# Kernel optimization log

Hardware: AMD Instinct MI355X
Metric: run time of the kernel (lower is better)

Reference implementation:

```python
import jax, jax.numpy as jnp
import numpy as np

G = 8            # tile grid (8x8)
BINS = 256
CLIP_LIMIT = 4.0
H = W = 4096


def setup_inputs() -> dict:
    key = jax.random.key(0)
    k1, k2 = jax.random.split(key)
    img = jax.random.uniform(k1, (3, H, W), dtype=jnp.float32)
    # torch code draws alpha ~ U(0.5, 1.0) per tile; we pass raw U(0,1) and rescale inside
    alphas = jax.random.uniform(k2, (G * G,), dtype=jnp.float32)
    return {"img": img, "alphas": alphas}


def _to_tiles(x, hs, ws):
    # [h, w] -> [G*G, hs, ws]
    return x.reshape(G, hs, G, ws).transpose(0, 2, 1, 3).reshape(G * G, hs, ws)


def _from_tiles(t, h, w, hs, ws):
    # [G*G, hs, ws] -> [h, w]
    return t.reshape(G, G, hs, ws).transpose(0, 2, 1, 3).reshape(h, w)


def reference(img, alphas):
    c, h, w = img.shape
    hs, ws = h // G, w // G
    n_tiles = G * G
    alpha = (0.5 + 0.5 * alphas)[:, None, None]  # U(0.5,1) per tile

    lum = jnp.mean(img, axis=0)                  # [h, w]
    tiles = _to_tiles(lum, hs, ws)               # [64, hs, ws]

    # per-tile 256-bin histogram over [0,1] (torch.histc semantics: v=1 -> last bin)
    bin_idx = jnp.clip((tiles * BINS).astype(jnp.int32), 0, BINS - 1)
    flat_idx = (jnp.arange(n_tiles, dtype=jnp.int32)[:, None, None] * BINS + bin_idx).reshape(-1)
    hist = jax.ops.segment_sum(
        jnp.ones(flat_idx.shape, jnp.float32), flat_idx, num_segments=n_tiles * BINS
    ).reshape(n_tiles, BINS)

    # clip + uniform redistribution of excess
    cl = float(max(1, int(CLIP_LIMIT * hs * ws / BINS)))
    excess = jnp.sum(jnp.maximum(hist - cl, 0.0), axis=1, keepdims=True)
    hist = jnp.minimum(hist, cl) + excess / BINS

    cdf = jnp.cumsum(hist, axis=1)
    cdf = cdf / cdf[:, -1:]                      # [64, 256]

    tmin = tiles.min(axis=(1, 2), keepdims=True)
    tmax = tiles.max(axis=(1, 2), keepdims=True)
    valid = tmin < tmax                          # [64, 1, 1]

    norm = (tiles - tmin) / jnp.where(valid, tmax - tmin, 1.0)
    idx = jnp.clip((norm * 255.0).astype(jnp.int32), 0, 255)
    enhanced = cdf[jnp.arange(n_tiles)[:, None, None], idx]   # gather remap
    enhanced = alpha * enhanced + (1.0 - alpha) * tiles

    enh_full = _from_tiles(enhanced, h, w, hs, ws)            # [h, w]
    valid_full = _from_tiles(jnp.broadcast_to(valid, (n_tiles, hs, ws)), h, w, hs, ws)

    # per-channel color ratio: img/lum where lum > 1e-5 else 1 (safe division)
    nz = lum > 1e-5
    safe_lum = jnp.where(nz, lum, 1.0)
    ratio = jnp.where(nz[None], img / safe_lum[None], 1.0)    # [3, h, w]

    out = jnp.where(valid_full[None], enh_full[None] * ratio, img)
    return jnp.clip(out, 0.0, 1.0)
```

## Files before the change

kernel.cpp:

```cpp
#include <hip/hip_runtime.h>

#define HH 4096
#define WW 4096
#define TS 512
#define NBINS 256
#define NT 64
#define NCHUNK 32
#define NBLK (NT * NCHUNK)
#define PLANE (HH * WW)

typedef float vf4 __attribute__((ext_vector_type(4)));

__device__ __forceinline__ float wred_min(float v) {
#pragma unroll
    for (int o = 32; o > 0; o >>= 1) v = fminf(v, __shfl_down(v, o, 64));
    return v;
}
__device__ __forceinline__ float wred_max(float v) {
#pragma unroll
    for (int o = 32; o > 0; o >>= 1) v = fmaxf(v, __shfl_down(v, o, 64));
    return v;
}
__device__ __forceinline__ float wred_sum(float v) {
#pragma unroll
    for (int o = 32; o > 0; o >>= 1) v += __shfl_down(v, o, 64);
    return v;
}


#define HIST_LANE(comp)                                              \
    {                                                                \
        float l = (a.comp + b.comp + c.comp) / 3.0f;                 \
        vmin = fminf(vmin, l);                                       \
        vmax = fmaxf(vmax, l);                                       \
        int bb = (int)(l * 256.0f);                                  \
        bb = bb < 0 ? 0 : (bb > 255 ? 255 : bb);                     \
        atomicAdd(&sh[bb], 1u);                                      \
    }

__global__ __launch_bounds__(256) void k_hist_p(const float* __restrict__ img,
                                                unsigned* __restrict__ part,
                                                float* __restrict__ pmin,
                                                float* __restrict__ pmax) {
    __shared__ unsigned sh0[NBINS], sh1[NBINS];
    __shared__ float smin[4], smax[4];
    int tid = threadIdx.x;
    sh0[tid] = 0u;
    sh1[tid] = 0u;
    __syncthreads();

    unsigned* sh = ((tid >> 6) & 1) ? sh1 : sh0;

    int bx = blockIdx.x;
    int t = bx >> 5;
    int chunk = bx & 31;
    int row0 = (t >> 3) * TS + chunk * 16;
    int cb4 = (t & 7) * (TS / 4);

    const float4* p0 = (const float4*)(img);
    const float4* p1 = (const float4*)(img + PLANE);
    const float4* p2 = (const float4*)(img + 2 * PLANE);

    int colv = tid & 127;
    int rsub = tid >> 7;
    float vmin = 1e30f, vmax = -1e30f;

#pragma unroll
    for (int it = 0; it < 8; ++it) {
        int r = row0 + (it << 1) + rsub;
        size_t idx4 = (size_t)r * (WW / 4) + cb4 + colv;
        float4 a = p0[idx4];
        float4 b = p1[idx4];
        float4 c = p2[idx4];
        HIST_LANE(x)
        HIST_LANE(y)
        HIST_LANE(z)
        HIST_LANE(w)
    }

    float wmn = wred_min(vmin), wmx = wred_max(vmax);
    if ((tid & 63) == 0) { smin[tid >> 6] = wmn; smax[tid >> 6] = wmx; }
    __syncthreads();
    if (tid == 0) {
        pmin[bx] = fminf(fminf(smin[0], smin[1]), fminf(smin[2], smin[3]));
        pmax[bx] = fmaxf(fmaxf(smax[0], smax[1]), fmaxf(smax[2], smax[3]));
    }
    part[(size_t)bx * NBINS + tid] = sh0[tid] + sh1[tid];
}

__global__ __launch_bounds__(256) void k_cdf_p(const unsigned* __restrict__ part,
                                               const float* __restrict__ pmin,
                                               const float* __restrict__ pmax,
                                               const float* __restrict__ alphas,
                                               float* __restrict__ cdfa,
                                               float* __restrict__ params) {
    __shared__ float wtot[4];
    __shared__ float wsums[4];
    __shared__ float sminmax[2];
    int t = blockIdx.x, tid = threadIdx.x;

    float h = 0.0f;
#pragma unroll
    for (int c = 0; c < NCHUNK; ++c)
        h += (float)part[((size_t)(t * NCHUNK + c)) * NBINS + tid];

    const float cl = 4096.0f;

    float ex = fmaxf(h - cl, 0.0f);
    float w = wred_sum(ex);
    if ((tid & 63) == 0) wsums[tid >> 6] = w;

    if (tid < 64) {
        float m = (tid < NCHUNK) ? pmin[t * NCHUNK + tid] : 1e30f;
        float M = (tid < NCHUNK) ? pmax[t * NCHUNK + tid] : -1e30f;
        m = wred_min(m);
        M = wred_max(M);
        if (tid == 0) { sminmax[0] = m; sminmax[1] = M; }
    }
    __syncthreads();
    float excess = wsums[0] + wsums[1] + wsums[2] + wsums[3];

    float hc = fminf(h, cl) + excess / 256.0f;

    int lane = tid & 63, wv = tid >> 6;
    float v = hc;
#pragma unroll
    for (int off = 1; off < 64; off <<= 1) {
        float u = __shfl_up(v, off, 64);
        if (lane >= off) v += u;
    }
    if (lane == 63) wtot[wv] = v;
    __syncthreads();
    float base = 0.0f;
    if (wv > 0) base += wtot[0];
    if (wv > 1) base += wtot[1];
    if (wv > 2) base += wtot[2];
    float cdf = base + v;
    float total = ((wtot[0] + wtot[1]) + wtot[2]) + wtot[3];

    float alpha = 0.5f + 0.5f * alphas[t];
    cdfa[t * NBINS + tid] = alpha * (cdf / total);

    if (tid == 0) {
        float tmin = sminmax[0];
        float tmax = sminmax[1];
        bool valid = tmin < tmax;
        params[t * 4 + 0] = tmin;
        params[t * 4 + 1] = valid ? (tmax - tmin) : 1.0f;
        params[t * 4 + 2] = 1.0f - alpha;
        params[t * 4 + 3] = valid ? 1.0f : 0.0f;
    }
}


__global__ __launch_bounds__(256) void k_hist_a(const float* __restrict__ img,
                                                unsigned* __restrict__ ghist,
                                                unsigned* __restrict__ minu,
                                                unsigned* __restrict__ maxu) {
    __shared__ unsigned sh[NBINS];
    __shared__ float smin[4], smax[4];
    int tid = threadIdx.x;
    sh[tid] = 0u;
    __syncthreads();
    unsigned* sh_ = sh;
#define sh sh_
    int bx = blockIdx.x;
    int t = bx >> 5;
    int chunk = bx & 31;
    int row0 = (t >> 3) * TS + chunk * 16;
    int cb4 = (t & 7) * (TS / 4);
    const float4* p0 = (const float4*)(img);
    const float4* p1 = (const float4*)(img + PLANE);
    const float4* p2 = (const float4*)(img + 2 * PLANE);
    int colv = tid & 127;
    int rsub = tid >> 7;
    float vmin = 1e30f, vmax = -1e30f;
#pragma unroll
    for (int it = 0; it < 8; ++it) {
        int r = row0 + (it << 1) + rsub;
        size_t idx4 = (size_t)r * (WW / 4) + cb4 + colv;
        float4 a = p0[idx4];
        float4 b = p1[idx4];
        float4 c = p2[idx4];
        HIST_LANE(x)
        HIST_LANE(y)
        HIST_LANE(z)
        HIST_LANE(w)
    }
#undef sh
    float wmn = wred_min(vmin), wmx = wred_max(vmax);
    if ((tid & 63) == 0) { smin[tid >> 6] = wmn; smax[tid >> 6] = wmx; }
    __syncthreads();
    if (tid == 0) {
        float m = fminf(fminf(smin[0], smin[1]), fminf(smin[2], smin[3]));
        float M = fmaxf(fmaxf(smax[0], smax[1]), fmaxf(smax[2], smax[3]));
        atomicMax(&minu[t], 0x3F800000u - __float_as_uint(m));
        atomicMax(&maxu[t], __float_as_uint(M));
    }
    atomicAdd(&ghist[t * NBINS + tid], sh_[tid]);
}

__global__ __launch_bounds__(256) void k_cdf_a(const unsigned* __restrict__ ghist,
                                               const unsigned* __restrict__ minu,
                                               const unsigned* __restrict__ maxu,
                                               const float* __restrict__ alphas,
                                               float* __restrict__ cdfa,
                                               float* __restrict__ params) {
    __shared__ float wtot[4];
    __shared__ float wsums[4];
    int t = blockIdx.x, tid = threadIdx.x;
    float h = (float)ghist[t * NBINS + tid];
    const float cl = 4096.0f;
    float ex = fmaxf(h - cl, 0.0f);
    float w = wred_sum(ex);
    if ((tid & 63) == 0) wsums[tid >> 6] = w;
    __syncthreads();
    float excess = wsums[0] + wsums[1] + wsums[2] + wsums[3];
    float hc = fminf(h, cl) + excess / 256.0f;

    int lane = tid & 63, wv = tid >> 6;
    float v = hc;
#pragma unroll
    for (int off = 1; off < 64; off <<= 1) {
        float u = __shfl_up(v, off, 64);
        if (lane >= off) v += u;
    }
    if (lane == 63) wtot[wv] = v;
    __syncthreads();
    float base = 0.0f;
    if (wv > 0) base += wtot[0];
    if (wv > 1) base += wtot[1];
    if (wv > 2) base += wtot[2];
    float cdf = base + v;
    float total = ((wtot[0] + wtot[1]) + wtot[2]) + wtot[3];

    float alpha = 0.5f + 0.5f * alphas[t];
    cdfa[t * NBINS + tid] = alpha * (cdf / total);

    if (tid == 0) {
        float tmin = __uint_as_float(0x3F800000u - minu[t]);
        float tmax = __uint_as_float(maxu[t]);
        bool valid = tmin < tmax;
        params[t * 4 + 0] = tmin;
        params[t * 4 + 1] = valid ? (tmax - tmin) : 1.0f;
        params[t * 4 + 2] = 1.0f - alpha;
        params[t * 4 + 3] = valid ? 1.0f : 0.0f;
    }
}


#define APPLY_LANE(comp)                                             \
    {                                                                \
        float l = (a.comp + b.comp + c.comp) / 3.0f;                 \
        float nrm = (l - tp.x) / tp.y;                               \
        int ix = (int)(nrm * 255.0f);                                \
        ix = ix < 0 ? 0 : (ix > 255 ? 255 : ix);                     \
        float enh = ct[ix] + tp.z * l;                               \
        float e0, e1, e2;                                            \
        if (l > 1e-5f) {                                             \
            float rinv = enh / l;                                    \
            e0 = a.comp * rinv;                                      \
            e1 = b.comp * rinv;                                      \
            e2 = c.comp * rinv;                                      \
        } else {                                                     \
            e0 = enh; e1 = enh; e2 = enh;                            \
        }                                                            \
        if (tp.w == 0.0f) { e0 = a.comp; e1 = b.comp; e2 = c.comp; } \
        r0.comp = fminf(fmaxf(e0, 0.0f), 1.0f);                      \
        r1.comp = fminf(fmaxf(e1, 0.0f), 1.0f);                      \
        r2.comp = fminf(fmaxf(e2, 0.0f), 1.0f);                      \
    }

__global__ __launch_bounds__(256) void k_apply(const float* __restrict__ img,
                                               float* __restrict__ out,
                                               const float* __restrict__ cdfa,
                                               const float* __restrict__ params) {
    const float4* p0 = (const float4*)(img);
    const float4* p1 = (const float4*)(img + PLANE);
    const float4* p2 = (const float4*)(img + 2 * PLANE);
    vf4* o0 = (vf4*)(out);
    vf4* o1 = (vf4*)(out + PLANE);
    vf4* o2 = (vf4*)(out + 2 * PLANE);

    const int nvec = PLANE / 4;
    int stride = gridDim.x * blockDim.x;
    for (int j = blockIdx.x * blockDim.x + threadIdx.x; j < nvec; j += stride) {
        int p = j << 2;
        int hh = p >> 12;
        int wq = p & 4095;
        int t = ((hh >> 9) << 3) | (wq >> 9);
        float4 tp = ((const float4*)params)[t];
        const float* ct = cdfa + (t << 8);

        float4 a = p0[j];
        float4 b = p1[j];
        float4 c = p2[j];
        float4 r0, r1, r2;
        APPLY_LANE(x)
        APPLY_LANE(y)
        APPLY_LANE(z)
        APPLY_LANE(w)
        vf4 v0 = {r0.x, r0.y, r0.z, r0.w};
        vf4 v1 = {r1.x, r1.y, r1.z, r1.w};
        vf4 v2 = {r2.x, r2.y, r2.z, r2.w};
        __builtin_nontemporal_store(v0, &o0[j]);
        __builtin_nontemporal_store(v1, &o1[j]);
        __builtin_nontemporal_store(v2, &o2[j]);
    }
}

extern "C" void kernel_launch(void* const* d_in, const int* in_sizes, int n_in,
                              void* d_out, int out_size, void* d_ws, size_t ws_size,
                              hipStream_t stream) {
    const float* img = (const float*)d_in[0];
    const float* alphas = (const float*)d_in[1];
    float* out = (float*)d_out;

    const size_t need = ((size_t)NBLK * NBINS + 2 * NBLK + NT * NBINS + NT * 4) * 4;

    if (ws_size >= need) {
        unsigned* part = (unsigned*)d_ws;
        float* pmin = (float*)(part + (size_t)NBLK * NBINS);
        float* pmax = pmin + NBLK;
        float* cdfa = pmax + NBLK;
        float* params = cdfa + NT * NBINS;

        k_hist_p<<<NBLK, 256, 0, stream>>>(img, part, pmin, pmax);
        k_cdf_p<<<NT, NBINS, 0, stream>>>(part, pmin, pmax, alphas, cdfa, params);
        k_apply<<<2048, 256, 0, stream>>>(img, out, cdfa, params);
    } else {
        unsigned* hist = (unsigned*)d_ws;
        unsigned* minu = hist + NT * NBINS;
        unsigned* maxu = minu + NT;
        float* cdfa = (float*)(maxu + 2 * NT);
        float* params = cdfa + NT * NBINS;

        (void)hipMemsetAsync(d_ws, 0, (size_t)(NT * NBINS + 3 * NT) * 4, stream);
        k_hist_a<<<NBLK, 256, 0, stream>>>(img, hist, minu, maxu);
        k_cdf_a<<<NT, NBINS, 0, stream>>>(hist, minu, maxu, alphas, cdfa, params);
        k_apply<<<2048, 256, 0, stream>>>(img, out, cdfa, params);
    }
}
```

Baseline: 96.55 us.

## Fuse CDF computation into tile-ordered apply kernel and use four shared histograms

Removes the separate per-tile CDF kernel. Each apply block now re-reduces its tile's 32 partial histograms, builds the clipped CDF in shared memory, and then processes the same 16-row chunk the histogram kernel covered. The histogram kernel uses four padded per-wave shared histograms instead of two, to reduce atomic contention. This saves one launch and the cdfa/params global round trip. The cost is that every block redundantly reads 32 KB of partial histograms, so the 64 CDF computations become 2048. The apply also switches to a fast reciprocal, which can change rounding slightly.

```diff
diff --git a/kernel.cpp b/kernel.cpp
--- a/kernel.cpp
+++ b/kernel.cpp
@@ -42,14 +42,16 @@
                                                 unsigned* __restrict__ part,
                                                 float* __restrict__ pmin,
                                                 float* __restrict__ pmax) {
-    __shared__ unsigned sh0[NBINS], sh1[NBINS];
+    __shared__ unsigned shh[4][NBINS + 1];
     __shared__ float smin[4], smax[4];
     int tid = threadIdx.x;
-    sh0[tid] = 0u;
-    sh1[tid] = 0u;
-    __syncthreads();
-
-    unsigned* sh = ((tid >> 6) & 1) ? sh1 : sh0;
+    shh[0][tid] = 0u;
+    shh[1][tid] = 0u;
+    shh[2][tid] = 0u;
+    shh[3][tid] = 0u;
+    __syncthreads();
+
+    unsigned* sh = shh[tid >> 6];
 
     int bx = blockIdx.x;
     int t = bx >> 5;
@@ -85,27 +87,53 @@
         pmin[bx] = fminf(fminf(smin[0], smin[1]), fminf(smin[2], smin[3]));
         pmax[bx] = fmaxf(fmaxf(smax[0], smax[1]), fmaxf(smax[2], smax[3]));
     }
-    part[(size_t)bx * NBINS + tid] = sh0[tid] + sh1[tid];
-}
-
-__global__ __launch_bounds__(256) void k_cdf_p(const unsigned* __restrict__ part,
-                                               const float* __restrict__ pmin,
-                                               const float* __restrict__ pmax,
-                                               const float* __restrict__ alphas,
-                                               float* __restrict__ cdfa,
-                                               float* __restrict__ params) {
+    part[(size_t)bx * NBINS + tid] =
+        shh[0][tid] + shh[1][tid] + shh[2][tid] + shh[3][tid];
+}
+
+#define APPLY_LANE2(comp)                                            \
+    {                                                                \
+        float l = (a.comp + b.comp + c.comp) / 3.0f;                 \
+        float nrm = (l - tmin) / den;                                \
+        int ix = (int)(nrm * 255.0f);                                \
+        ix = ix < 0 ? 0 : (ix > 255 ? 255 : ix);                     \
+        float enh = sc[ix] + oma * l;                                \
+        float e0, e1, e2;                                            \
+        if (l > 1e-5f) {                                             \
+            float rinv = enh * __builtin_amdgcn_rcpf(l);             \
+            e0 = a.comp * rinv;                                      \
+            e1 = b.comp * rinv;                                      \
+            e2 = c.comp * rinv;                                      \
+        } else {                                                     \
+            e0 = enh; e1 = enh; e2 = enh;                            \
+        }                                                            \
+        if (vflag == 0.0f) { e0 = a.comp; e1 = b.comp; e2 = c.comp; }\
+        r0.comp = fminf(fmaxf(e0, 0.0f), 1.0f);                      \
+        r1.comp = fminf(fmaxf(e1, 0.0f), 1.0f);                      \
+        r2.comp = fminf(fmaxf(e2, 0.0f), 1.0f);                      \
+    }
+
+__global__ __launch_bounds__(256) void k_apply_t(const float* __restrict__ img,
+                                                 float* __restrict__ out,
+                                                 const unsigned* __restrict__ part,
+                                                 const float* __restrict__ pmin,
+                                                 const float* __restrict__ pmax,
+                                                 const float* __restrict__ alphas) {
+    __shared__ float sc[NBINS];
     __shared__ float wtot[4];
     __shared__ float wsums[4];
-    __shared__ float sminmax[2];
-    int t = blockIdx.x, tid = threadIdx.x;
+    __shared__ float sp[4];
+    int tid = threadIdx.x;
+    int bx = blockIdx.x;
+    int t = bx >> 5;
+    int chunk = bx & 31;
 
     float h = 0.0f;
 #pragma unroll
     for (int c = 0; c < NCHUNK; ++c)
-        h += (float)part[((size_t)(t * NCHUNK + c)) * NBINS + tid];
+        h += (float)part[(((size_t)(t * NCHUNK + c)) << 8) + tid];
 
     const float cl = 4096.0f;
-
     float ex = fmaxf(h - cl, 0.0f);
     float w = wred_sum(ex);
     if ((tid & 63) == 0) wsums[tid >> 6] = w;
@@ -115,11 +143,17 @@
         float M = (tid < NCHUNK) ? pmax[t * NCHUNK + tid] : -1e30f;
         m = wred_min(m);
         M = wred_max(M);
-        if (tid == 0) { sminmax[0] = m; sminmax[1] = M; }
+        if (tid == 0) {
+            float alpha = 0.5f + 0.5f * alphas[t];
+            bool valid = m < M;
+            sp[0] = m;
+            sp[1] = valid ? (M - m) : 1.0f;
+            sp[2] = 1.0f - alpha;
+            sp[3] = valid ? 1.0f : 0.0f;
+        }
     }
     __syncthreads();
     float excess = wsums[0] + wsums[1] + wsums[2] + wsums[3];
-
     float hc = fminf(h, cl) + excess / 256.0f;
 
     int lane = tid & 63, wv = tid >> 6;
@@ -139,16 +173,42 @@
     float total = ((wtot[0] + wtot[1]) + wtot[2]) + wtot[3];
 
     float alpha = 0.5f + 0.5f * alphas[t];
-    cdfa[t * NBINS + tid] = alpha * (cdf / total);
-
-    if (tid == 0) {
-        float tmin = sminmax[0];
-        float tmax = sminmax[1];
-        bool valid = tmin < tmax;
-        params[t * 4 + 0] = tmin;
-        params[t * 4 + 1] = valid ? (tmax - tmin) : 1.0f;
-        params[t * 4 + 2] = 1.0f - alpha;
-        params[t * 4 + 3] = valid ? 1.0f : 0.0f;
+    sc[tid] = alpha * (cdf / total);
+    __syncthreads();
+
+    float tmin = sp[0], den = sp[1], oma = sp[2], vflag = sp[3];
+
+    int row0 = (t >> 3) * TS + chunk * 16;
+    int cb4 = (t & 7) * (TS / 4);
+
+    const float4* p0 = (const float4*)(img);
+    const float4* p1 = (const float4*)(img + PLANE);
+    const float4* p2 = (const float4*)(img + 2 * PLANE);
+    vf4* o0 = (vf4*)(out);
+    vf4* o1 = (vf4*)(out + PLANE);
+    vf4* o2 = (vf4*)(out + 2 * PLANE);
+
+    int colv = tid & 127;
+    int rsub = tid >> 7;
+
+#pragma unroll
+    for (int it = 0; it < 8; ++it) {
+        int r = row0 + (it << 1) + rsub;
+        size_t idx4 = (size_t)r * (WW / 4) + cb4 + colv;
+        float4 a = p0[idx4];
+        float4 b = p1[idx4];
+        float4 c = p2[idx4];
+        float4 r0, r1, r2;
+        APPLY_LANE2(x)
+        APPLY_LANE2(y)
+        APPLY_LANE2(z)
+        APPLY_LANE2(w)
+        vf4 v0 = {r0.x, r0.y, r0.z, r0.w};
+        vf4 v1 = {r1.x, r1.y, r1.z, r1.w};
+        vf4 v2 = {r2.x, r2.y, r2.z, r2.w};
+        __builtin_nontemporal_store(v0, &o0[idx4]);
+        __builtin_nontemporal_store(v1, &o1[idx4]);
+        __builtin_nontemporal_store(v2, &o2[idx4]);
     }
 }
 
@@ -157,13 +217,12 @@
                                                 unsigned* __restrict__ ghist,
                                                 unsigned* __restrict__ minu,
                                                 unsigned* __restrict__ maxu) {
-    __shared__ unsigned sh[NBINS];
+    __shared__ unsigned shf[NBINS];
     __shared__ float smin[4], smax[4];
     int tid = threadIdx.x;
-    sh[tid] = 0u;
-    __syncthreads();
-    unsigned* sh_ = sh;
-#define sh sh_
+    shf[tid] = 0u;
+    __syncthreads();
+    unsigned* sh = shf;
     int bx = blockIdx.x;
     int t = bx >> 5;
     int chunk = bx & 31;
@@ -187,7 +246,6 @@
         HIST_LANE(z)
         HIST_LANE(w)
     }
-#undef sh
     float wmn = wred_min(vmin), wmx = wred_max(vmax);
     if ((tid & 63) == 0) { smin[tid >> 6] = wmn; smax[tid >> 6] = wmx; }
     __syncthreads();
@@ -197,7 +255,7 @@
         atomicMax(&minu[t], 0x3F800000u - __float_as_uint(m));
         atomicMax(&maxu[t], __float_as_uint(M));
     }
-    atomicAdd(&ghist[t * NBINS + tid], sh_[tid]);
+    atomicAdd(&ghist[t * NBINS + tid], shf[tid]);
 }
 
 __global__ __launch_bounds__(256) void k_cdf_a(const unsigned* __restrict__ ghist,
@@ -247,7 +305,6 @@
         params[t * 4 + 3] = valid ? 1.0f : 0.0f;
     }
 }
-
 
 #define APPLY_LANE(comp)                                             \
     {                                                                \
@@ -271,10 +328,10 @@
         r2.comp = fminf(fmaxf(e2, 0.0f), 1.0f);                      \
     }
 
-__global__ __launch_bounds__(256) void k_apply(const float* __restrict__ img,
-                                               float* __restrict__ out,
-                                               const float* __restrict__ cdfa,
-                                               const float* __restrict__ params) {
+__global__ __launch_bounds__(256) void k_apply_flat(const float* __restrict__ img,
+                                                    float* __restrict__ out,
+                                                    const float* __restrict__ cdfa,
+                                                    const float* __restrict__ params) {
     const float4* p0 = (const float4*)(img);
     const float4* p1 = (const float4*)(img + PLANE);
     const float4* p2 = (const float4*)(img + 2 * PLANE);
@@ -316,18 +373,15 @@
     const float* alphas = (const float*)d_in[1];
     float* out = (float*)d_out;
 
-    const size_t need = ((size_t)NBLK * NBINS + 2 * NBLK + NT * NBINS + NT * 4) * 4;
+    const size_t need = ((size_t)NBLK * NBINS + 2 * NBLK) * 4;
 
     if (ws_size >= need) {
         unsigned* part = (unsigned*)d_ws;
         float* pmin = (float*)(part + (size_t)NBLK * NBINS);
         float* pmax = pmin + NBLK;
-        float* cdfa = pmax + NBLK;
-        float* params = cdfa + NT * NBINS;
 
         k_hist_p<<<NBLK, 256, 0, stream>>>(img, part, pmin, pmax);
-        k_cdf_p<<<NT, NBINS, 0, stream>>>(part, pmin, pmax, alphas, cdfa, params);
-        k_apply<<<2048, 256, 0, stream>>>(img, out, cdfa, params);
+        k_apply_t<<<NBLK, 256, 0, stream>>>(img, out, part, pmin, pmax, alphas);
     } else {
         unsigned* hist = (unsigned*)d_ws;
         unsigned* minu = hist + NT * NBINS;
@@ -338,6 +392,6 @@
         (void)hipMemsetAsync(d_ws, 0, (size_t)(NT * NBINS + 3 * NT) * 4, stream);
         k_hist_a<<<NBLK, 256, 0, stream>>>(img, hist, minu, maxu);
         k_cdf_a<<<NT, NBINS, 0, stream>>>(hist, minu, maxu, alphas, cdfa, params);
-        k_apply<<<2048, 256, 0, stream>>>(img, out, cdfa, params);
-    }
-}
+        k_apply_flat<<<2048, 256, 0, stream>>>(img, out, cdfa, params);
+    }
+}
```

Result: slower. 100.8 us (+4.4%).

## Tile-aligned apply kernel with LDS CDF table, per-wave histograms, rcp division

Applied to the files above, without the earlier changes.

The apply pass now assigns each block to one tile chunk, matching the histogram pass. Each block loads that tile's CDF and parameters into LDS once, so the per-pixel tile index computation and global gathers go away. Division by luminance uses a hardware reciprocal approximation, which may differ slightly in the last bits from exact division. The histogram kernel now gives each wave its own padded LDS histogram instead of two shared ones, which reduces atomic contention at the cost of more shared memory.

```diff
diff --git a/kernel.cpp b/kernel.cpp
--- a/kernel.cpp
+++ b/kernel.cpp
@@ -27,7 +27,6 @@
     return v;
 }
 
-
 #define HIST_LANE(comp)                                              \
     {                                                                \
         float l = (a.comp + b.comp + c.comp) / 3.0f;                 \
@@ -42,14 +41,16 @@
                                                 unsigned* __restrict__ part,
                                                 float* __restrict__ pmin,
                                                 float* __restrict__ pmax) {
-    __shared__ unsigned sh0[NBINS], sh1[NBINS];
+    __shared__ unsigned shh[4][NBINS + 1];
     __shared__ float smin[4], smax[4];
     int tid = threadIdx.x;
-    sh0[tid] = 0u;
-    sh1[tid] = 0u;
-    __syncthreads();
-
-    unsigned* sh = ((tid >> 6) & 1) ? sh1 : sh0;
+    shh[0][tid] = 0u;
+    shh[1][tid] = 0u;
+    shh[2][tid] = 0u;
+    shh[3][tid] = 0u;
+    __syncthreads();
+
+    unsigned* sh = shh[tid >> 6];
 
     int bx = blockIdx.x;
     int t = bx >> 5;
@@ -85,7 +86,8 @@
         pmin[bx] = fminf(fminf(smin[0], smin[1]), fminf(smin[2], smin[3]));
         pmax[bx] = fmaxf(fmaxf(smax[0], smax[1]), fmaxf(smax[2], smax[3]));
     }
-    part[(size_t)bx * NBINS + tid] = sh0[tid] + sh1[tid];
+    part[(size_t)bx * NBINS + tid] =
+        shh[0][tid] + shh[1][tid] + shh[2][tid] + shh[3][tid];
 }
 
 __global__ __launch_bounds__(256) void k_cdf_p(const unsigned* __restrict__ part,
@@ -152,18 +154,90 @@
     }
 }
 
+#define APPLY_LANE2(comp)                                            \
+    {                                                                \
+        float l = (a.comp + b.comp + c.comp) / 3.0f;                 \
+        float nrm = (l - tmin) / den;                                \
+        int ix = (int)(nrm * 255.0f);                                \
+        ix = ix < 0 ? 0 : (ix > 255 ? 255 : ix);                     \
+        float enh = sc[ix] + oma * l;                                \
+        float e0, e1, e2;                                            \
+        if (l > 1e-5f) {                                             \
+            float rinv = enh * __builtin_amdgcn_rcpf(l);             \
+            e0 = a.comp * rinv;                                      \
+            e1 = b.comp * rinv;                                      \
+            e2 = c.comp * rinv;                                      \
+        } else {                                                     \
+            e0 = enh; e1 = enh; e2 = enh;                            \
+        }                                                            \
+        if (vflag == 0.0f) { e0 = a.comp; e1 = b.comp; e2 = c.comp; }\
+        r0.comp = fminf(fmaxf(e0, 0.0f), 1.0f);                      \
+        r1.comp = fminf(fmaxf(e1, 0.0f), 1.0f);                      \
+        r2.comp = fminf(fmaxf(e2, 0.0f), 1.0f);                      \
+    }
+
+__global__ __launch_bounds__(256) void k_apply_t(const float* __restrict__ img,
+                                                 float* __restrict__ out,
+                                                 const float* __restrict__ cdfa,
+                                                 const float* __restrict__ params) {
+    __shared__ float sc[NBINS];
+    __shared__ float sp[4];
+    int tid = threadIdx.x;
+    int bx = blockIdx.x;
+    int t = bx >> 5;
+    int chunk = bx & 31;
+
+    sc[tid] = cdfa[(t << 8) + tid];
+    if (tid < 4) sp[tid] = params[(t << 2) + tid];
+    __syncthreads();
+
+    float tmin = sp[0], den = sp[1], oma = sp[2], vflag = sp[3];
+
+    int row0 = (t >> 3) * TS + chunk * 16;
+    int cb4 = (t & 7) * (TS / 4);
+
+    const float4* p0 = (const float4*)(img);
+    const float4* p1 = (const float4*)(img + PLANE);
+    const float4* p2 = (const float4*)(img + 2 * PLANE);
+    vf4* o0 = (vf4*)(out);
+    vf4* o1 = (vf4*)(out + PLANE);
+    vf4* o2 = (vf4*)(out + 2 * PLANE);
+
+    int colv = tid & 127;
+    int rsub = tid >> 7;
+
+#pragma unroll
+    for (int it = 0; it < 8; ++it) {
+        int r = row0 + (it << 1) + rsub;
+        size_t idx4 = (size_t)r * (WW / 4) + cb4 + colv;
+        float4 a = p0[idx4];
+        float4 b = p1[idx4];
+        float4 c = p2[idx4];
+        float4 r0, r1, r2;
+        APPLY_LANE2(x)
+        APPLY_LANE2(y)
+        APPLY_LANE2(z)
+        APPLY_LANE2(w)
+        vf4 v0 = {r0.x, r0.y, r0.z, r0.w};
+        vf4 v1 = {r1.x, r1.y, r1.z, r1.w};
+        vf4 v2 = {r2.x, r2.y, r2.z, r2.w};
+        __builtin_nontemporal_store(v0, &o0[idx4]);
+        __builtin_nontemporal_store(v1, &o1[idx4]);
+        __builtin_nontemporal_store(v2, &o2[idx4]);
+    }
+}
+
 
 __global__ __launch_bounds__(256) void k_hist_a(const float* __restrict__ img,
                                                 unsigned* __restrict__ ghist,
                                                 unsigned* __restrict__ minu,
                                                 unsigned* __restrict__ maxu) {
-    __shared__ unsigned sh[NBINS];
+    __shared__ unsigned shf[NBINS];
     __shared__ float smin[4], smax[4];
     int tid = threadIdx.x;
-    sh[tid] = 0u;
-    __syncthreads();
-    unsigned* sh_ = sh;
-#define sh sh_
+    shf[tid] = 0u;
+    __syncthreads();
+    unsigned* sh = shf;
     int bx = blockIdx.x;
     int t = bx >> 5;
     int chunk = bx & 31;
@@ -187,7 +261,6 @@
         HIST_LANE(z)
         HIST_LANE(w)
     }
-#undef sh
     float wmn = wred_min(vmin), wmx = wred_max(vmax);
     if ((tid & 63) == 0) { smin[tid >> 6] = wmn; smax[tid >> 6] = wmx; }
     __syncthreads();
@@ -197,7 +270,7 @@
         atomicMax(&minu[t], 0x3F800000u - __float_as_uint(m));
         atomicMax(&maxu[t], __float_as_uint(M));
     }
-    atomicAdd(&ghist[t * NBINS + tid], sh_[tid]);
+    atomicAdd(&ghist[t * NBINS + tid], shf[tid]);
 }
 
 __global__ __launch_bounds__(256) void k_cdf_a(const unsigned* __restrict__ ghist,
@@ -248,67 +321,6 @@
     }
 }
 
-
-#define APPLY_LANE(comp)                                             \
-    {                                                                \
-        float l = (a.comp + b.comp + c.comp) / 3.0f;                 \
-        float nrm = (l - tp.x) / tp.y;                               \
-        int ix = (int)(nrm * 255.0f);                                \
-        ix = ix < 0 ? 0 : (ix > 255 ? 255 : ix);                     \
-        float enh = ct[ix] + tp.z * l;                               \
-        float e0, e1, e2;                                            \
-        if (l > 1e-5f) {                                             \
-            float rinv = enh / l;                                    \
-            e0 = a.comp * rinv;                                      \
-            e1 = b.comp * rinv;                                      \
-            e2 = c.comp * rinv;                                      \
-        } else {                                                     \
-            e0 = enh; e1 = enh; e2 = enh;                            \
-        }                                                            \
-        if (tp.w == 0.0f) { e0 = a.comp; e1 = b.comp; e2 = c.comp; } \
-        r0.comp = fminf(fmaxf(e0, 0.0f), 1.0f);                      \
-        r1.comp = fminf(fmaxf(e1, 0.0f), 1.0f);                      \
-        r2.comp = fminf(fmaxf(e2, 0.0f), 1.0f);                      \
-    }
-
-__global__ __launch_bounds__(256) void k_apply(const float* __restrict__ img,
-                                               float* __restrict__ out,
-                                               const float* __restrict__ cdfa,
-                                               const float* __restrict__ params) {
-    const float4* p0 = (const float4*)(img);
-    const float4* p1 = (const float4*)(img + PLANE);
-    const float4* p2 = (const float4*)(img + 2 * PLANE);
-    vf4* o0 = (vf4*)(out);
-    vf4* o1 = (vf4*)(out + PLANE);
-    vf4* o2 = (vf4*)(out + 2 * PLANE);
-
-    const int nvec = PLANE / 4;
-    int stride = gridDim.x * blockDim.x;
-    for (int j = blockIdx.x * blockDim.x + threadIdx.x; j < nvec; j += stride) {
-        int p = j << 2;
-        int hh = p >> 12;
-        int wq = p & 4095;
-        int t = ((hh >> 9) << 3) | (wq >> 9);
-        float4 tp = ((const float4*)params)[t];
-        const float* ct = cdfa + (t << 8);
-
-        float4 a = p0[j];
-        float4 b = p1[j];
-        float4 c = p2[j];
-        float4 r0, r1, r2;
-        APPLY_LANE(x)
-        APPLY_LANE(y)
-        APPLY_LANE(z)
-        APPLY_LANE(w)
-        vf4 v0 = {r0.x, r0.y, r0.z, r0.w};
-        vf4 v1 = {r1.x, r1.y, r1.z, r1.w};
-        vf4 v2 = {r2.x, r2.y, r2.z, r2.w};
-        __builtin_nontemporal_store(v0, &o0[j]);
-        __builtin_nontemporal_store(v1, &o1[j]);
-        __builtin_nontemporal_store(v2, &o2[j]);
-    }
-}
-
 extern "C" void kernel_launch(void* const* d_in, const int* in_sizes, int n_in,
                               void* d_out, int out_size, void* d_ws, size_t ws_size,
                               hipStream_t stream) {
@@ -327,7 +339,7 @@
 
         k_hist_p<<<NBLK, 256, 0, stream>>>(img, part, pmin, pmax);
         k_cdf_p<<<NT, NBINS, 0, stream>>>(part, pmin, pmax, alphas, cdfa, params);
-        k_apply<<<2048, 256, 0, stream>>>(img, out, cdfa, params);
+        k_apply_t<<<NBLK, 256, 0, stream>>>(img, out, cdfa, params);
     } else {
         unsigned* hist = (unsigned*)d_ws;
         unsigned* minu = hist + NT * NBINS;
@@ -338,6 +350,6 @@
         (void)hipMemsetAsync(d_ws, 0, (size_t)(NT * NBINS + 3 * NT) * 4, stream);
         k_hist_a<<<NBLK, 256, 0, stream>>>(img, hist, minu, maxu);
         k_cdf_a<<<NT, NBINS, 0, stream>>>(hist, minu, maxu, alphas, cdfa, params);
-        k_apply<<<2048, 256, 0, stream>>>(img, out, cdfa, params);
-    }
-}
+        k_apply_t<<<NBLK, 256, 0, stream>>>(img, out, cdfa, params);
+    }
+}
```

Result: no change. 96.72 us, median of 2 (+0.2%).
